# Kernel tuning notes

Measured on AMD Instinct MI355X. Metric: run time of the kernel, lower is better.

## Reference

```python
import jax, jax.numpy as jnp
import numpy as np

B, N, P, K = 4, 8192, 2048, 16
C_IN, C_OUT, DIMS = 64, 128, 3
C_MID = C_OUT // 4                      # 32 (C_in != 0 branch)
DM = min(int(np.ceil(C_OUT / C_IN)), 4) # 2, depth multiplier for SepConv
C_DENSE = C_OUT // 2                    # 64, dense-projected feature dim
C_CAT = C_MID + C_DENSE                 # 96, lifted + projected features


def setup_inputs() -> dict:
    key = jax.random.key(0)
    ks = jax.random.split(key, 12)
    g = lambda k, shape, fan: jax.random.normal(k, shape, jnp.float32) / np.sqrt(fan).astype(np.float32)
    return {
        "pts": jax.random.normal(ks[0], (B, N, DIMS), jnp.float32),
        "fts": jax.random.normal(ks[1], (B, N, C_IN), jnp.float32),
        # PointCNN.dense: Linear(C_in, C_out//2) + ELU
        "dense_W": g(ks[2], (C_IN, C_DENSE), C_IN), "dense_b": jnp.zeros((C_DENSE,), jnp.float32),
        # XConv.dense1/dense2: Linear(dims,C_mid)+ELU, Linear(C_mid,C_mid)+ELU
        "d1_W": g(ks[3], (DIMS, C_MID), DIMS), "d1_b": jnp.zeros((C_MID,), jnp.float32),
        "d2_W": g(ks[4], (C_MID, C_MID), C_MID), "d2_b": jnp.zeros((C_MID,), jnp.float32),
        # conv2d: Conv2d(dims, K*K, (1,K)) + ELU, weight (out, in, kW)
        "conv_W": g(ks[5], (K * K, DIMS, K), DIMS * K), "conv_b": jnp.zeros((K * K,), jnp.float32),
        # dep_conv1/2: depthwise Conv2d(K, K*K, (1,K), groups=K); weight (group, mult, kW)
        "dw1_W": g(ks[6], (K, K, K), K), "dw1_b": jnp.zeros((K, K), jnp.float32),
        "dw2_W": g(ks[7], (K, K, K), K), "dw2_b": jnp.zeros((K, K), jnp.float32),
        # end_conv SepConv: depthwise (C_CAT groups, DM mult, (1,K)) then pointwise 1x1 -> C_OUT, ELU
        "sep_dw_W": g(ks[8], (C_CAT, DM, K), K), "sep_dw_b": jnp.zeros((C_CAT, DM), jnp.float32),
        "sep_pw_W": g(ks[9], (C_OUT, C_CAT, DM), C_CAT * DM), "sep_pw_b": jnp.zeros((C_OUT,), jnp.float32),
    }


def _fps(pts, npoint):
    """Iterative farthest point sampling (deterministic start at index 0)."""
    b, n, _ = pts.shape
    dist0 = jnp.full((b, n), 1e10, pts.dtype)
    far0 = jnp.zeros((b,), jnp.int32)

    def step(carry, _):
        dist, far = carry
        centroid = jnp.take_along_axis(pts, far[:, None, None], axis=1)  # [B,1,3]
        d = jnp.sum((pts - centroid) ** 2, -1)                            # [B,N]
        dist = jnp.minimum(dist, d)
        return (dist, jnp.argmax(dist, -1).astype(jnp.int32)), far

    _, idx = jax.lax.scan(step, (dist0, far0), None, length=npoint)  # [P,B]
    idx = idx.T                                                       # [B,P]
    return jnp.take_along_axis(pts, idx[..., None], axis=1)          # [B,P,3]


def reference(pts, fts, dense_W, dense_b, d1_W, d1_b, d2_W, d2_b,
              conv_W, conv_b, dw1_W, dw1_b, dw2_W, dw2_b,
              sep_dw_W, sep_dw_b, sep_pw_W, sep_pw_b):
    rep_pts = _fps(pts, P)                                            # [B,P,3]
    fts_d = jax.nn.elu(fts @ dense_W + dense_b)                       # [B,N,64]
    # KNN: squared distances rep->all points, K smallest
    d2 = (jnp.sum(rep_pts ** 2, -1)[..., None]
          - 2.0 * jnp.einsum('npc,nqc->npq', rep_pts, pts)
          + jnp.sum(pts ** 2, -1)[:, None, :])                        # [B,P,N]
    _, idx = jax.lax.top_k(-d2, K)                                    # [B,P,K]
    bidx = jnp.arange(B)[:, None, None]
    pts_reg = pts[bidx, idx]                                          # [B,P,K,3]
    fts_reg = fts_d[bidx, idx]                                        # [B,P,K,64]
    # XConv
    pl = pts_reg - rep_pts[:, :, None, :]                             # local coords
    lift = jax.nn.elu(jax.nn.elu(pl @ d1_W + d1_b) @ d2_W + d2_b)     # [B,P,K,C_MID]
    fts_cat = jnp.concatenate([lift, fts_reg], -1)                    # [B,P,K,C_CAT]
    X = jax.nn.elu(jnp.einsum('npkc,ock->npo', pl, conv_W) + conv_b).reshape(B, P, K, K)
    # depthwise convs over neighbor axis (spatial dim collapses to 1 -> einsum)
    X = jax.nn.elu(jnp.einsum('npij,jmi->npjm', X, dw1_W) + dw1_b)
    X = jnp.einsum('npij,jmi->npjm', X, dw2_W) + dw2_b
    fts_X = jnp.einsum('npab,npbc->npac', X, fts_cat)                 # [B,P,K,C_CAT]
    # separable end conv: depthwise over K, pointwise to C_OUT, ELU
    d = jnp.einsum('npkc,cmk->npcm', fts_X, sep_dw_W) + sep_dw_b
    fts_p = jax.nn.elu(jnp.einsum('npcm,ocm->npo', d, sep_pw_W) + sep_pw_b)  # [B,P,C_OUT]
    return rep_pts, fts_p
```

## Files before the change

### kernel.cpp

```cpp
#include <hip/hip_runtime.h>

#define BB 4
#define NN 8192
#define PP 2048
#define KNB 16
#define CIN 64
#define COUT 128

__device__ __forceinline__ float elu(float x) { return x > 0.0f ? x : expm1f(x); }

__device__ __forceinline__ unsigned fkey(float d) {
    unsigned u = __float_as_uint(d);
    unsigned m = (unsigned)((int)u >> 31);
    return u ^ (m | 0x80000000u);
}

__global__ __launch_bounds__(256) void fps_kernel(const float* __restrict__ pts,
                                                  float* __restrict__ rep) {
    const int b = blockIdx.x;
    const int t = threadIdx.x;
    const int lane = t & 63, wave = t >> 6;

    __shared__ float spx[NN];
    __shared__ float spy[NN];
    __shared__ float spz[NN];
    __shared__ unsigned long long partk[2][4];

    const float* pb = pts + (size_t)b * NN * 3;
    for (int i = t; i < NN; i += 256) {
        spx[i] = pb[3 * i + 0];
        spy[i] = pb[3 * i + 1];
        spz[i] = pb[3 * i + 2];
    }
    __syncthreads();

    float px[32], py[32], pz[32], dist[32];
#pragma unroll
    for (int r = 0; r < 32; ++r) {
        px[r] = spx[t * 32 + r];
        py[r] = spy[t * 32 + r];
        pz[r] = spz[t * 32 + r];
        dist[r] = 1e10f;
    }

    float cx = spx[0], cy = spy[0], cz = spz[0];
    if (t == 0) {
        rep[(size_t)b * PP * 3 + 0] = cx;
        rep[(size_t)b * PP * 3 + 1] = cy;
        rep[(size_t)b * PP * 3 + 2] = cz;
    }

    int buf = 0;
    for (int s = 1; s < PP; ++s) {
        float bv = -1.0f; int bi = 0;
#pragma unroll
        for (int r = 0; r < 32; ++r) {
            float dx = __fsub_rn(px[r], cx);
            float dy = __fsub_rn(py[r], cy);
            float dz = __fsub_rn(pz[r], cz);
            float d = __fadd_rn(__fadd_rn(__fmul_rn(dx, dx), __fmul_rn(dy, dy)), __fmul_rn(dz, dz));
            float nd = fminf(dist[r], d);
            dist[r] = nd;
            bool tk = nd > bv;
            bi = tk ? (t * 32 + r) : bi;
            bv = fmaxf(nd, bv);
        }

        float wmax = bv;
#pragma unroll
        for (int off = 32; off >= 1; off >>= 1)
            wmax = fmaxf(wmax, __shfl_xor(wmax, off));
        unsigned long long mask = __ballot(bv == wmax);
        int wl = __ffsll(mask) - 1;
        int wbi = __shfl(bi, wl);

        if (lane == 0)
            partk[buf][wave] = ((unsigned long long)__float_as_uint(wmax) << 32)
                             | (unsigned)(8191 - wbi);
        __syncthreads();

        unsigned long long kk = partk[buf][0];
#pragma unroll
        for (int q = 1; q < 4; ++q) {
            unsigned long long c = partk[buf][q];
            kk = c > kk ? c : kk;
        }
        int widx = 8191 - (int)(unsigned)(kk & 0xFFFFFFFFULL);
        cx = spx[widx]; cy = spy[widx]; cz = spz[widx];
        if (t == 0) {
            float* rp = rep + ((size_t)b * PP + s) * 3;
            rp[0] = cx; rp[1] = cy; rp[2] = cz;
        }
        buf ^= 1;
    }
}

__global__ __launch_bounds__(256) void prep_kernel(
    const float* __restrict__ convW, const float* __restrict__ dw1W,
    const float* __restrict__ dw2W, const float* __restrict__ sdwW,
    const float* __restrict__ spwW,
    float* __restrict__ convT, float* __restrict__ dw1T, float* __restrict__ dw2T,
    float* __restrict__ sdwT, float* __restrict__ spwT) {
    int i = blockIdx.x * 256 + threadIdx.x;
    if (i < 12288) {
        int k = i & 15, c = (i >> 4) % 3, o = i / 48;
        convT[(c * 16 + k) * 256 + o] = convW[i];
    }
    if (i < 4096) {
        int ii = i & 15, e = i >> 4;
        dw1T[ii * 256 + e] = dw1W[i];
        dw2T[ii * 256 + e] = dw2W[i];
    }
    if (i < 3072) {
        int k = i & 15, e = i >> 4;
        sdwT[k * 192 + e] = sdwW[i];
    }
    if (i < 24576) {
        int e2 = i % 192, o = i / 192;
        spwT[e2 * 128 + o] = spwW[i];
    }
}

__global__ __launch_bounds__(256) void dense_kernel(const float* __restrict__ fts,
                                                    const float* __restrict__ W,
                                                    const float* __restrict__ bias,
                                                    float* __restrict__ out) {
    const int row = blockIdx.x * 4 + (threadIdx.x >> 6);
    const int c = threadIdx.x & 63;
    float v = fts[(size_t)row * 64 + c];
    float acc = bias[c];
#pragma unroll 8
    for (int k = 0; k < 64; ++k) acc = fmaf(__shfl(v, k), W[k * 64 + c], acc);
    out[(size_t)row * 64 + c] = elu(acc);
}

__global__ __launch_bounds__(256) void knn_kernel(const float* __restrict__ pts,
                                                  const float* __restrict__ rep,
                                                  int* __restrict__ kidx) {
    const int wid = blockIdx.x * 4 + (threadIdx.x >> 6);
    const int lane = threadIdx.x & 63;
    const int b = wid >> 11;
    const float* pb = pts + (size_t)b * NN * 3;

    float rx = rep[(size_t)wid * 3 + 0];
    float ry = rep[(size_t)wid * 3 + 1];
    float rz = rep[(size_t)wid * 3 + 2];
    float a = __fadd_rn(__fadd_rn(__fmul_rn(rx, rx), __fmul_rn(ry, ry)), __fmul_rn(rz, rz));

    unsigned long long key[16];
#pragma unroll
    for (int s = 0; s < 16; ++s) key[s] = ~0ULL;

    for (int j = lane; j < NN; j += 64) {
        float qx = pb[j * 3 + 0], qy = pb[j * 3 + 1], qz = pb[j * 3 + 2];
        float cc = __fadd_rn(__fadd_rn(__fmul_rn(qx, qx), __fmul_rn(qy, qy)), __fmul_rn(qz, qz));
        float bs = __fadd_rn(__fadd_rn(__fmul_rn(rx, qx), __fmul_rn(ry, qy)), __fmul_rn(rz, qz));
        float d2 = __fadd_rn(__fsub_rn(a, __fmul_rn(2.0f, bs)), cc);
        unsigned long long nk = ((unsigned long long)fkey(d2) << 32) | (unsigned)j;
        if (nk < key[15]) {
            key[15] = nk;
#pragma unroll
            for (int s2 = 15; s2 > 0; --s2) {
                unsigned long long u = key[s2 - 1], w = key[s2];
                bool sw = w < u;
                key[s2 - 1] = sw ? w : u;
                key[s2] = sw ? u : w;
            }
        }
    }

    int outv = 0;
#pragma unroll 1
    for (int r = 0; r < 16; ++r) {
        unsigned long long h = key[0];
#pragma unroll
        for (int off = 1; off < 64; off <<= 1) {
            unsigned long long o = __shfl_xor(h, off);
            h = (o < h) ? o : h;
        }
        if (lane == r) outv = (int)(unsigned)(h & 0xFFFFFFFFull);
        if (key[0] == h) {
#pragma unroll
            for (int s2 = 0; s2 < 15; ++s2) key[s2] = key[s2 + 1];
            key[15] = ~0ULL;
        }
    }
    if (lane < 16) kidx[(size_t)wid * 16 + lane] = outv;
}

__global__ __launch_bounds__(128) void xconv_kernel(
    const float* __restrict__ pts, const float* __restrict__ rep,
    const float* __restrict__ ftsd, const int* __restrict__ kidx,
    const float* __restrict__ d1W, const float* __restrict__ d1b,
    const float* __restrict__ d2W, const float* __restrict__ d2b,
    const float* __restrict__ convT, const float* __restrict__ convb,
    const float* __restrict__ dw1T, const float* __restrict__ dw1b,
    const float* __restrict__ dw2T, const float* __restrict__ dw2b,
    const float* __restrict__ sdwT, const float* __restrict__ sdwb,
    const float* __restrict__ spwT, const float* __restrict__ spwb,
    float* __restrict__ outp) {
    const int bp = blockIdx.x;
    const int b = bp >> 11;
    const int t = threadIdx.x;
    const int c64 = t & 63;

    __shared__ float pl[16][3];
    __shared__ int nidx[16];
    __shared__ float fcat[16][96];
    __shared__ float A1[16][32];
    __shared__ float Xm[16][17];
    __shared__ float X2[16][17];
    __shared__ float X3[16][17];
    __shared__ float fX[16][97];
    __shared__ float dsep[192];

    if (t < 16) {
        int id = kidx[(size_t)bp * 16 + t];
        nidx[t] = id;
        const float* q = pts + ((size_t)b * NN + id) * 3;
        const float* rr = rep + (size_t)bp * 3;
        pl[t][0] = q[0] - rr[0];
        pl[t][1] = q[1] - rr[1];
        pl[t][2] = q[2] - rr[2];
    }
    __syncthreads();

#pragma unroll
    for (int it = 0; it < 8; ++it) {
        int k = (t >> 6) + it * 2;
        fcat[k][32 + c64] = ftsd[((size_t)b * NN + nidx[k]) * 64 + c64];
    }

#pragma unroll
    for (int r2 = 0; r2 < 4; ++r2) {
        int e = t + 128 * r2; int k = e >> 5, j = e & 31;
        float acc = d1b[j];
        acc = fmaf(pl[k][0], d1W[j], acc);
        acc = fmaf(pl[k][1], d1W[32 + j], acc);
        acc = fmaf(pl[k][2], d1W[64 + j], acc);
        A1[k][j] = elu(acc);
    }
    __syncthreads();

#pragma unroll
    for (int r2 = 0; r2 < 4; ++r2) {
        int e = t + 128 * r2; int k = e >> 5, j = e & 31;
        float acc = d2b[j];
#pragma unroll
        for (int c = 0; c < 32; ++c) acc = fmaf(A1[k][c], d2W[c * 32 + j], acc);
        fcat[k][j] = elu(acc);
    }
    __syncthreads();

    {
        float a0 = convb[t], a1 = convb[t + 128];
#pragma unroll
        for (int c = 0; c < 3; ++c)
#pragma unroll
            for (int k = 0; k < 16; ++k) {
                float p = pl[k][c];
                const float* w = convT + (c * 16 + k) * 256 + t;
                a0 = fmaf(p, w[0],   a0);
                a1 = fmaf(p, w[128], a1);
            }
        Xm[t >> 4][t & 15] = elu(a0);
        Xm[(t >> 4) + 8][t & 15] = elu(a1);
    }
    __syncthreads();

    {
        int m = t & 15, j0 = t >> 4;
        float a0 = dw1b[t], a1 = dw1b[t + 128];
#pragma unroll
        for (int i = 0; i < 16; ++i) {
            const float* w = dw1T + i * 256 + t;
            a0 = fmaf(Xm[i][j0],     w[0],   a0);
            a1 = fmaf(Xm[i][j0 + 8], w[128], a1);
        }
        X2[j0][m] = elu(a0); X2[j0 + 8][m] = elu(a1);
    }
    __syncthreads();

    {
        int m = t & 15, j0 = t >> 4;
        float a0 = dw2b[t], a1 = dw2b[t + 128];
#pragma unroll
        for (int i = 0; i < 16; ++i) {
            const float* w = dw2T + i * 256 + t;
            a0 = fmaf(X2[i][j0],     w[0],   a0);
            a1 = fmaf(X2[i][j0 + 8], w[128], a1);
        }
        X3[j0][m] = a0; X3[j0 + 8][m] = a1;
    }
    __syncthreads();

#pragma unroll
    for (int r2 = 0; r2 < 12; ++r2) {
        int e = t + 128 * r2; int a = e & 15, c = e >> 4;
        float acc = 0.0f;
#pragma unroll
        for (int q = 0; q < 16; ++q) acc = fmaf(X3[a][q], fcat[q][c], acc);
        fX[a][c] = acc;
    }
    __syncthreads();

#pragma unroll
    for (int r2 = 0; r2 < 2; ++r2) {
        int e = t + 128 * r2;
        if (e < 192) {
            int c = e >> 1;
            float acc = sdwb[e];
#pragma unroll
            for (int k = 0; k < 16; ++k) acc = fmaf(fX[k][c], sdwT[k * 192 + e], acc);
            dsep[e] = acc;
        }
    }
    __syncthreads();

    {
        float a0 = spwb[t];
#pragma unroll 16
        for (int e2 = 0; e2 < 192; ++e2)
            a0 = fmaf(dsep[e2], spwT[e2 * 128 + t], a0);
        outp[(size_t)bp * 128 + t] = elu(a0);
    }
}

extern "C" void kernel_launch(void* const* d_in, const int* in_sizes, int n_in,
                              void* d_out, int out_size, void* d_ws, size_t ws_size,
                              hipStream_t stream) {
    const float* pts    = (const float*)d_in[0];
    const float* fts    = (const float*)d_in[1];
    const float* denseW = (const float*)d_in[2];
    const float* denseb = (const float*)d_in[3];
    const float* d1W    = (const float*)d_in[4];
    const float* d1b    = (const float*)d_in[5];
    const float* d2W    = (const float*)d_in[6];
    const float* d2b    = (const float*)d_in[7];
    const float* convW  = (const float*)d_in[8];
    const float* convb  = (const float*)d_in[9];
    const float* dw1W   = (const float*)d_in[10];
    const float* dw1b   = (const float*)d_in[11];
    const float* dw2W   = (const float*)d_in[12];
    const float* dw2b   = (const float*)d_in[13];
    const float* sdwW   = (const float*)d_in[14];
    const float* sdwb   = (const float*)d_in[15];
    const float* spwW   = (const float*)d_in[16];
    const float* spwb   = (const float*)d_in[17];

    float* rep  = (float*)d_out;
    float* outp = (float*)d_out + (size_t)BB * PP * 3;

    float* ftsd = (float*)d_ws;
    int*   kidx = (int*)((char*)d_ws + (size_t)BB * NN * CIN * sizeof(float));
    float* wts  = (float*)((char*)d_ws + (size_t)BB * NN * CIN * sizeof(float)
                                       + (size_t)BB * PP * KNB * sizeof(int));
    float* convT = wts;
    float* dw1T  = wts + 12288;
    float* dw2T  = wts + 16384;
    float* sdwT  = wts + 20480;
    float* spwT  = wts + 23552;

    prep_kernel<<<96, 256, 0, stream>>>(convW, dw1W, dw2W, sdwW, spwW,
                                        convT, dw1T, dw2T, sdwT, spwT);
    dense_kernel<<<BB * NN / 4, 256, 0, stream>>>(fts, denseW, denseb, ftsd);
    fps_kernel<<<BB, 256, 0, stream>>>(pts, rep);
    knn_kernel<<<BB * PP / 4, 256, 0, stream>>>(pts, rep, kidx);
    xconv_kernel<<<BB * PP, 128, 0, stream>>>(pts, rep, ftsd, kidx,
                                              d1W, d1b, d2W, d2b, convT, convb,
                                              dw1T, dw1b, dw2T, dw2b,
                                              sdwT, sdwb, spwT, spwb, outp);
}
```

Measured before the change: 2.665 ms.

## Fuse prep and dense into FPS launch, widen FPS blocks, use DPP reduction

The FPS kernel is widened to 512 threads, so each thread holds 16 points instead of 32, and its wave max reduction now uses DPP row operations instead of shuffles. The weight-prep and dense-projection work is folded into the same launch as extra blocks, so it runs alongside the serial 4-block FPS instead of before it. Those blocks also write a structure-of-arrays copy of the points, which KNN now reads for coalesced loads. The cost is more waves taking part in each per-step barrier, larger shared-memory reduction state, and a workspace buffer that must fit in the allocated space.

```diff
diff --git a/kernel.cpp b/kernel.cpp
--- a/kernel.cpp
+++ b/kernel.cpp
@@ -15,31 +15,99 @@
     return u ^ (m | 0x80000000u);
 }
 
-__global__ __launch_bounds__(256) void fps_kernel(const float* __restrict__ pts,
-                                                  float* __restrict__ rep) {
-    const int b = blockIdx.x;
+__device__ __forceinline__ float wave_max_dpp(float v) {
+#define DPP_STEP(ctrl)                                                         \
+    {                                                                          \
+        int x = __float_as_int(v);                                             \
+        int y = __builtin_amdgcn_update_dpp(x, x, (ctrl), 0xf, 0xf, false);    \
+        v = fmaxf(v, __int_as_float(y));                                       \
+    }
+    DPP_STEP(0x111)
+    DPP_STEP(0x112)
+    DPP_STEP(0x114)
+    DPP_STEP(0x118)
+    DPP_STEP(0x142)
+    DPP_STEP(0x143)
+#undef DPP_STEP
+    return __int_as_float(__builtin_amdgcn_readlane(__float_as_int(v), 63));
+}
+
+#define PREP_BLOCKS 64
+#define DENSE_BASE (4 + PREP_BLOCKS)
+#define TOTAL_BLOCKS (DENSE_BASE + BB * NN / 8)
+
+__global__ __launch_bounds__(512) void fps_kernel(
+    const float* __restrict__ pts, float* __restrict__ rep,
+    const float* __restrict__ fts, const float* __restrict__ denseW,
+    const float* __restrict__ denseb, float* __restrict__ ftsd,
+    const float* __restrict__ convW, const float* __restrict__ dw1W,
+    const float* __restrict__ dw2W, const float* __restrict__ sdwW,
+    const float* __restrict__ spwW,
+    float* __restrict__ convT, float* __restrict__ dw1T, float* __restrict__ dw2T,
+    float* __restrict__ sdwT, float* __restrict__ spwT, float* __restrict__ ptsT) {
+    const int bid = blockIdx.x;
     const int t = threadIdx.x;
-    const int lane = t & 63, wave = t >> 6;
 
     __shared__ float spx[NN];
     __shared__ float spy[NN];
     __shared__ float spz[NN];
-    __shared__ unsigned long long partk[2][4];
+    __shared__ unsigned long long partk[2][8];
+
+    if (bid >= DENSE_BASE) {
+        const int row = (bid - DENSE_BASE) * 8 + (t >> 6);
+        const int c = t & 63;
+        float v = fts[(size_t)row * 64 + c];
+        float acc = denseb[c];
+#pragma unroll 8
+        for (int k = 0; k < 64; ++k) acc = fmaf(__shfl(v, k), denseW[k * 64 + c], acc);
+        ftsd[(size_t)row * 64 + c] = elu(acc);
+        return;
+    }
+    if (bid >= 4) {
+        int i = (bid - 4) * 512 + t;
+        if (i < 12288) {
+            int k = i & 15, c = (i >> 4) % 3, o = i / 48;
+            convT[(c * 16 + k) * 256 + o] = convW[i];
+        }
+        if (i < 4096) {
+            int ii = i & 15, e = i >> 4;
+            dw1T[ii * 256 + e] = dw1W[i];
+            dw2T[ii * 256 + e] = dw2W[i];
+        }
+        if (i < 3072) {
+            int k = i & 15, e = i >> 4;
+            sdwT[k * 192 + e] = sdwW[i];
+        }
+        if (i < 24576) {
+            int e2 = i % 192, o = i / 192;
+            spwT[e2 * 128 + o] = spwW[i];
+        }
+        {
+            int j = i & 8191, b2 = i >> 13;
+#pragma unroll
+            for (int d = 0; d < 3; ++d)
+                ptsT[((size_t)b2 * 3 + d) * NN + j] = pts[((size_t)b2 * NN + j) * 3 + d];
+        }
+        return;
+    }
+
+    const int b = bid;
+    const int lane = t & 63, wave = t >> 6;
 
     const float* pb = pts + (size_t)b * NN * 3;
-    for (int i = t; i < NN; i += 256) {
+    for (int i = t; i < NN; i += 512) {
         spx[i] = pb[3 * i + 0];
         spy[i] = pb[3 * i + 1];
         spz[i] = pb[3 * i + 2];
     }
     __syncthreads();
 
-    float px[32], py[32], pz[32], dist[32];
-#pragma unroll
-    for (int r = 0; r < 32; ++r) {
-        px[r] = spx[t * 32 + r];
-        py[r] = spy[t * 32 + r];
-        pz[r] = spz[t * 32 + r];
+    float px[16], py[16], pz[16], dist[16];
+#pragma unroll
+    for (int r = 0; r < 16; ++r) {
+        px[r] = spx[t * 16 + r];
+        py[r] = spy[t * 16 + r];
+        pz[r] = spz[t * 16 + r];
         dist[r] = 1e10f;
     }
 
@@ -54,7 +122,7 @@
     for (int s = 1; s < PP; ++s) {
         float bv = -1.0f; int bi = 0;
 #pragma unroll
-        for (int r = 0; r < 32; ++r) {
+        for (int r = 0; r < 16; ++r) {
             float dx = __fsub_rn(px[r], cx);
             float dy = __fsub_rn(py[r], cy);
             float dz = __fsub_rn(pz[r], cz);
@@ -62,14 +130,11 @@
             float nd = fminf(dist[r], d);
             dist[r] = nd;
             bool tk = nd > bv;
-            bi = tk ? (t * 32 + r) : bi;
+            bi = tk ? (t * 16 + r) : bi;
             bv = fmaxf(nd, bv);
         }
 
-        float wmax = bv;
-#pragma unroll
-        for (int off = 32; off >= 1; off >>= 1)
-            wmax = fmaxf(wmax, __shfl_xor(wmax, off));
+        float wmax = wave_max_dpp(bv);
         unsigned long long mask = __ballot(bv == wmax);
         int wl = __ffsll(mask) - 1;
         int wbi = __shfl(bi, wl);
@@ -81,7 +146,7 @@
 
         unsigned long long kk = partk[buf][0];
 #pragma unroll
-        for (int q = 1; q < 4; ++q) {
+        for (int q = 1; q < 8; ++q) {
             unsigned long long c = partk[buf][q];
             kk = c > kk ? c : kk;
         }
@@ -95,52 +160,15 @@
     }
 }
 
-__global__ __launch_bounds__(256) void prep_kernel(
-    const float* __restrict__ convW, const float* __restrict__ dw1W,
-    const float* __restrict__ dw2W, const float* __restrict__ sdwW,
-    const float* __restrict__ spwW,
-    float* __restrict__ convT, float* __restrict__ dw1T, float* __restrict__ dw2T,
-    float* __restrict__ sdwT, float* __restrict__ spwT) {
-    int i = blockIdx.x * 256 + threadIdx.x;
-    if (i < 12288) {
-        int k = i & 15, c = (i >> 4) % 3, o = i / 48;
-        convT[(c * 16 + k) * 256 + o] = convW[i];
-    }
-    if (i < 4096) {
-        int ii = i & 15, e = i >> 4;
-        dw1T[ii * 256 + e] = dw1W[i];
-        dw2T[ii * 256 + e] = dw2W[i];
-    }
-    if (i < 3072) {
-        int k = i & 15, e = i >> 4;
-        sdwT[k * 192 + e] = sdwW[i];
-    }
-    if (i < 24576) {
-        int e2 = i % 192, o = i / 192;
-        spwT[e2 * 128 + o] = spwW[i];
-    }
-}
-
-__global__ __launch_bounds__(256) void dense_kernel(const float* __restrict__ fts,
-                                                    const float* __restrict__ W,
-                                                    const float* __restrict__ bias,
-                                                    float* __restrict__ out) {
-    const int row = blockIdx.x * 4 + (threadIdx.x >> 6);
-    const int c = threadIdx.x & 63;
-    float v = fts[(size_t)row * 64 + c];
-    float acc = bias[c];
-#pragma unroll 8
-    for (int k = 0; k < 64; ++k) acc = fmaf(__shfl(v, k), W[k * 64 + c], acc);
-    out[(size_t)row * 64 + c] = elu(acc);
-}
-
-__global__ __launch_bounds__(256) void knn_kernel(const float* __restrict__ pts,
+__global__ __launch_bounds__(256) void knn_kernel(const float* __restrict__ ptsT,
                                                   const float* __restrict__ rep,
                                                   int* __restrict__ kidx) {
     const int wid = blockIdx.x * 4 + (threadIdx.x >> 6);
     const int lane = threadIdx.x & 63;
     const int b = wid >> 11;
-    const float* pb = pts + (size_t)b * NN * 3;
+    const float* pxT = ptsT + (size_t)b * 3 * NN;
+    const float* pyT = pxT + NN;
+    const float* pzT = pxT + 2 * NN;
 
     float rx = rep[(size_t)wid * 3 + 0];
     float ry = rep[(size_t)wid * 3 + 1];
@@ -152,7 +180,7 @@
     for (int s = 0; s < 16; ++s) key[s] = ~0ULL;
 
     for (int j = lane; j < NN; j += 64) {
-        float qx = pb[j * 3 + 0], qy = pb[j * 3 + 1], qz = pb[j * 3 + 2];
+        float qx = pxT[j], qy = pyT[j], qz = pzT[j];
         float cc = __fadd_rn(__fadd_rn(__fmul_rn(qx, qx), __fmul_rn(qy, qy)), __fmul_rn(qz, qz));
         float bs = __fadd_rn(__fadd_rn(__fmul_rn(rx, qx), __fmul_rn(ry, qy)), __fmul_rn(rz, qz));
         float d2 = __fadd_rn(__fsub_rn(a, __fmul_rn(2.0f, bs)), cc);
@@ -360,12 +388,12 @@
     float* dw2T  = wts + 16384;
     float* sdwT  = wts + 20480;
     float* spwT  = wts + 23552;
-
-    prep_kernel<<<96, 256, 0, stream>>>(convW, dw1W, dw2W, sdwW, spwW,
-                                        convT, dw1T, dw2T, sdwT, spwT);
-    dense_kernel<<<BB * NN / 4, 256, 0, stream>>>(fts, denseW, denseb, ftsd);
-    fps_kernel<<<BB, 256, 0, stream>>>(pts, rep);
-    knn_kernel<<<BB * PP / 4, 256, 0, stream>>>(pts, rep, kidx);
+    float* ptsT  = wts + 48128;
+
+    fps_kernel<<<TOTAL_BLOCKS, 512, 0, stream>>>(pts, rep, fts, denseW, denseb, ftsd,
+                                                 convW, dw1W, dw2W, sdwW, spwW,
+                                                 convT, dw1T, dw2T, sdwT, spwT, ptsT);
+    knn_kernel<<<BB * PP / 4, 256, 0, stream>>>(ptsT, rep, kidx);
     xconv_kernel<<<BB * PP, 128, 0, stream>>>(pts, rep, ftsd, kidx,
                                               d1W, d1b, d2W, d2b, convT, convb,
                                               dw1T, dw1b, dw2T, dw2b,
```

Measured after the change: 2.264 ms. -15.0%, faster.
